# Optimization experiments

Hardware: AMD Instinct MI355X
Metric: run time of the kernel (lower is better)

Reference implementation:

```python
import jax, jax.numpy as jnp
import numpy as np

N_EMBD = 2048
N_HEAD = 16
HEAD_SIZE = N_EMBD // N_HEAD


def setup_inputs() -> dict:
    key = jax.random.key(0)
    k1, k2, k3 = jax.random.split(key, 3)
    x = jax.random.normal(k1, (4, 2048, N_EMBD), dtype=jnp.float32)
    # Linear weights stored as (in, out) for x @ W
    scale = 1.0 / np.sqrt(N_EMBD)
    w_qkv = jax.random.normal(k2, (N_EMBD, 3 * N_EMBD), dtype=jnp.float32) * scale
    w_proj = jax.random.normal(k3, (N_EMBD, N_EMBD), dtype=jnp.float32) * scale
    return {"x": x, "w_qkv": w_qkv, "w_proj": w_proj}


def reference(x, w_qkv, w_proj):
    B, T, C = x.shape
    qkv = x @ w_qkv  # [B, T, 3C]
    q, k, v = jnp.split(qkv, 3, axis=-1)
    # [B, H, T, Dh]
    def heads(t):
        return t.reshape(B, T, N_HEAD, HEAD_SIZE).transpose(0, 2, 1, 3)
    q, k, v = heads(q), heads(k), heads(v)
    scores = jnp.einsum('bhqd,bhkd->bhqk', q, k) * (1.0 / np.sqrt(HEAD_SIZE))
    causal = jnp.tril(jnp.ones((T, T), dtype=bool))
    scores = jnp.where(causal, scores, jnp.finfo(scores.dtype).min)
    att = jax.nn.softmax(scores, axis=-1)
    y = jnp.einsum('bhqk,bhkd->bhqd', att, v)
    y = y.transpose(0, 2, 1, 3).reshape(B, T, C)
    return y @ w_proj
```

## Files before the change

kernel.cpp:

```cpp
#include <hip/hip_runtime.h>

typedef unsigned short u16;
typedef unsigned int u32;
typedef __bf16 bf16x8 __attribute__((ext_vector_type(8)));
typedef float f32x4 __attribute__((ext_vector_type(4)));
typedef u32 u32x4 __attribute__((ext_vector_type(4)));

__device__ __forceinline__ u16 f2bf(float f) {
  u32 u = __builtin_bit_cast(u32, f);
  return (u16)((u + 0x7fffu + ((u >> 16) & 1u)) >> 16);
}

__device__ __forceinline__ f32x4 mfma16(bf16x8 a, bf16x8 b, f32x4 c) {
  return __builtin_amdgcn_mfma_f32_16x16x32_bf16(a, b, c, 0, 0, 0);
}

__device__ __forceinline__ u32 cvtpk_bf16(float lo, float hi) {
  u32 r;
  asm("v_cvt_pk_bf16_f32 %0, %1, %2" : "=v"(r) : "v"(lo), "v"(hi));
  return r;
}

struct alignas(8) U16x4 { u16 x, y, z, w; };

#define AS1 __attribute__((address_space(1)))
#define AS3 __attribute__((address_space(3)))
__device__ __forceinline__ void gl16(const u16* g, u16* l) {
  __builtin_amdgcn_global_load_lds((const AS1 u32*)g, (AS3 u32*)l, 16, 0, 0);
}

__global__ __launch_bounds__(256) void k_f32_to_bf16(const float* __restrict__ in,
                                                     u16* __restrict__ out, long n4) {
  long i = (long)blockIdx.x * blockDim.x + threadIdx.x;
  long stride = (long)gridDim.x * blockDim.x;
  for (; i < n4; i += stride) {
    float4 v = ((const float4*)in)[i];
    U16x4 o{f2bf(v.x), f2bf(v.y), f2bf(v.z), f2bf(v.w)};
    ((U16x4*)out)[i] = o;
  }
}

__global__ __launch_bounds__(256) void k_transpose_f32_to_bf16(const float* __restrict__ in,
                                                               u16* __restrict__ out,
                                                               int rows, int cols) {
  __shared__ float tile[32][33];
  int bc = blockIdx.x * 32, br = blockIdx.y * 32;
  int tx = threadIdx.x, ty = threadIdx.y;
  for (int i = 0; i < 32; i += 8)
    tile[ty + i][tx] = in[(long)(br + ty + i) * cols + bc + tx];
  __syncthreads();
  for (int i = 0; i < 32; i += 8)
    out[(long)(bc + ty + i) * rows + br + tx] = f2bf(tile[tx][ty + i]);
}

__global__ __launch_bounds__(256) void k_transpose_v(const u16* __restrict__ qkv,
                                                     u16* __restrict__ vt) {
  __shared__ u16 tile[32][33];
  int bh = blockIdx.z; int b = bh >> 4, h = bh & 15;
  int t0 = blockIdx.y * 32, d0 = blockIdx.x * 32;
  int tx = threadIdx.x, ty = threadIdx.y;
  const u16* src = qkv + (long)(b * 2048) * 6144 + 4096 + h * 128;
  for (int i = 0; i < 32; i += 8)
    tile[ty + i][tx] = src[(long)(t0 + ty + i) * 6144 + d0 + tx];
  __syncthreads();
  u16* dst = vt + (long)bh * 128 * 2048;
  for (int i = 0; i < 32; i += 8)
    dst[(long)(d0 + ty + i) * 2048 + t0 + tx] = tile[tx][ty + i];
}

template <typename OutT>
__global__ __launch_bounds__(512, 2) void k_gemm256(const u16* __restrict__ A,
                                                    const u16* __restrict__ Bt,
                                                    OutT* __restrict__ C,
                                                    int M, int N, int K) {
  __shared__ alignas(16) u16 As[4][8192];
  __shared__ alignas(16) u16 Bs[4][8192];

  int gx = gridDim.x;
  int nwg = gx * gridDim.y;
  int bid = blockIdx.y * gx + blockIdx.x;
  int swz = (bid & 7) * (nwg >> 3) + (bid >> 3);
  int rem = swz % (gx * 4);
  int bx = rem >> 2;
  int by = (swz / (gx * 4)) * 4 + (rem & 3);

  int tid = threadIdx.x;
  int lane = tid & 63;
  int w = tid >> 6;
  int wr = w >> 2, wc = w & 3;
  int lr = lane & 15, lg = lane >> 4;
  long brow = (long)by * 256, bcol = (long)bx * 256;

  int rS[2], cS[2];
#pragma unroll
  for (int i = 0; i < 2; ++i) {
    int q = i * 512 + tid;
    rS[i] = q >> 2;
    cS[i] = ((q & 3) ^ ((rS[i] >> 1) & 3)) << 3;
  }
  const u16* Ab = A + brow * K;
  const u16* Bb = Bt + bcol * K;

  int offA[8], offB[4];
#pragma unroll
  for (int m = 0; m < 8; ++m) {
    int row = wr * 128 + m * 16 + lr;
    offA[m] = row * 32 + ((lg ^ ((row >> 1) & 3)) << 3);
  }
#pragma unroll
  for (int n = 0; n < 4; ++n) {
    int row = wc * 64 + n * 16 + lr;
    offB[n] = row * 32 + ((lg ^ ((row >> 1) & 3)) << 3);
  }

  f32x4 zero = {0.f, 0.f, 0.f, 0.f};
  f32x4 acc[8][4];
#pragma unroll
  for (int m = 0; m < 8; ++m)
#pragma unroll
    for (int n = 0; n < 4; ++n) acc[m][n] = zero;

  int NS = K >> 5;

#define STAGE256(SBUF, KT)                                                          \
  do {                                                                              \
    int kk_ = (KT) << 5;                                                            \
    gl16(Ab + (long)rS[0] * K + kk_ + cS[0], &As[SBUF][(0 * 512 + w * 64) * 8]);    \
    gl16(Ab + (long)rS[1] * K + kk_ + cS[1], &As[SBUF][(1 * 512 + w * 64) * 8]);    \
    gl16(Bb + (long)rS[0] * K + kk_ + cS[0], &Bs[SBUF][(0 * 512 + w * 64) * 8]);    \
    gl16(Bb + (long)rS[1] * K + kk_ + cS[1], &Bs[SBUF][(1 * 512 + w * 64) * 8]);    \
  } while (0)

  STAGE256(0, 0);
  STAGE256(1, 1);
  STAGE256(2, 2);
  asm volatile("s_waitcnt vmcnt(8)" ::: "memory");
  __builtin_amdgcn_s_barrier();

  for (int s = 0; s < NS; ++s) {
    int cb = s & 3;
    bf16x8 af[8], bfn[4];
#pragma unroll
    for (int m = 0; m < 8; ++m) af[m] = *(const bf16x8*)&As[cb][offA[m]];
#pragma unroll
    for (int n = 0; n < 4; ++n) bfn[n] = *(const bf16x8*)&Bs[cb][offB[n]];
    int t = s + 3;
    int tb = t & 3;
    if (t > NS - 1) t = NS - 1;
    STAGE256(tb, t);
    __builtin_amdgcn_s_setprio(1);
#pragma unroll
    for (int m = 0; m < 4; ++m)
#pragma unroll
      for (int n = 0; n < 4; ++n) acc[m][n] = mfma16(af[m], bfn[n], acc[m][n]);
    __builtin_amdgcn_s_setprio(0);
    __builtin_amdgcn_s_setprio(1);
#pragma unroll
    for (int m = 4; m < 8; ++m)
#pragma unroll
      for (int n = 0; n < 4; ++n) acc[m][n] = mfma16(af[m], bfn[n], acc[m][n]);
    __builtin_amdgcn_s_setprio(0);
    asm volatile("s_waitcnt vmcnt(8)" ::: "memory");
    __builtin_amdgcn_s_barrier();
  }
#undef STAGE256
  asm volatile("s_waitcnt vmcnt(0)" ::: "memory");

#pragma unroll
  for (int m = 0; m < 8; ++m)
#pragma unroll
    for (int n = 0; n < 4; ++n)
#pragma unroll
      for (int r = 0; r < 4; ++r) {
        long row = brow + wr * 128 + m * 16 + lg * 4 + r;
        long col = bcol + wc * 64 + n * 16 + lr;
        float v = acc[m][n][r];
        if constexpr (sizeof(OutT) == 2)
          C[row * N + col] = (OutT)f2bf(v);
        else
          C[row * N + col] = v;
      }
}

__global__ __launch_bounds__(256, 2) void k_attn2(const u16* __restrict__ qkv,
                                                  const u16* __restrict__ vt,
                                                  u16* __restrict__ y) {
  __shared__ alignas(16) u16 Ks[2][64 * 128];
  __shared__ alignas(16) u16 Vs[2][128 * 64];

  int bh = blockIdx.x;
  int qb = 15 - (int)blockIdx.y;
  int b = bh >> 4, h = bh & 15;
  int tid = threadIdx.x;
  int lane = tid & 63;
  int w = tid >> 6;
  int lr = lane & 15, lg = lane >> 4;
  int x7 = lr & 7;
  bool hiA = (lane & 32) != 0;
  bool hiB = (lane & 16) != 0;
  const float scale = 0.08838834764831845f;

  const u16* kbase = qkv + (long)(b * 2048) * 6144 + 2048 + h * 128;
  const u16* vtbh = vt + (long)bh * 128 * 2048;
  int qbase = qb * 128 + w * 32;

  const u16* qptr = qkv + (long)(qb * 128 + b * 2048) * 6144 + h * 128;
  bf16x8 qf[2][4];
  for (int qsub = 0; qsub < 2; ++qsub)
    for (int dc = 0; dc < 4; ++dc)
      qf[qsub][dc] = *(const bf16x8*)(qptr + (long)(w * 32 + qsub * 16 + lr) * 6144 + dc * 32 + lg * 8);

  f32x4 zero = {0.f, 0.f, 0.f, 0.f};
  f32x4 o[2][8];
  for (int qs = 0; qs < 2; ++qs)
    for (int ds = 0; ds < 8; ++ds) o[qs][ds] = zero;
  float m_run[2] = {-1e30f, -1e30f};
  float l_run[2] = {0.f, 0.f};

  int nkt = 2 * qb + 2;
  int qmaxw = qbase + 31;

#define STAGE(BUF, KT)                                                          \
  do {                                                                          \
    for (int i_ = 0; i_ < 4; ++i_) {                                            \
      int rl_ = w * 16 + i_ * 4;                                                \
      int row_ = rl_ + (lane >> 4);                                             \
      int ch_ = (lane & 15) ^ (row_ & 7);                                       \
      gl16(kbase + (long)((KT)*64 + row_) * 6144 + ch_ * 8, &Ks[BUF][rl_ * 128]); \
    }                                                                           \
    for (int i_ = 0; i_ < 4; ++i_) {                                            \
      int dl_ = w * 32 + i_ * 8;                                                \
      int d_ = dl_ + (lane >> 3);                                               \
      int ch_ = (lane & 7) ^ (d_ & 7);                                          \
      gl16(vtbh + (long)d_ * 2048 + (KT)*64 + ch_ * 8, &Vs[BUF][dl_ * 64]);     \
    }                                                                           \
  } while (0)

#define COMPUTE(BUF, KT)                                                        \
  do {                                                                          \
    const u16* Kb = &Ks[BUF][0];                                                \
    const u16* Vb = &Vs[BUF][0];                                                \
    f32x4 s[2][4];                                                              \
    for (int qs = 0; qs < 2; ++qs)                                              \
      for (int ks = 0; ks < 4; ++ks) s[qs][ks] = zero;                          \
    for (int ks = 0; ks < 4; ++ks) {                                            \
      int row = ks * 16 + lr;                                                   \
      for (int dc = 0; dc < 4; ++dc) {                                          \
        bf16x8 kf = *(const bf16x8*)(Kb + row * 128 + ((dc * 4 + lg) ^ x7) * 8); \
        s[0][ks] = mfma16(kf, qf[0][dc], s[0][ks]);                             \
        s[1][ks] = mfma16(kf, qf[1][dc], s[1][ks]);                             \
      }                                                                         \
    }                                                                           \
    bf16x8 pa[2][2];                                                            \
    for (int qs = 0; qs < 2; ++qs) {                                            \
      int qg = qbase + qs * 16 + lr;                                            \
      float p[16];                                                              \
      float tmax = -1e30f;                                                      \
      for (int ks = 0; ks < 4; ++ks)                                            \
        for (int r = 0; r < 4; ++r) {                                           \
          int key = (KT)*64 + ks * 16 + lg * 4 + r;                             \
          float v = (key <= qg) ? s[qs][ks][r] * scale : -1e30f;                \
          p[ks * 4 + r] = v;                                                    \
          tmax = fmaxf(tmax, v);                                                \
        }                                                                       \
      tmax = fmaxf(tmax, __shfl_xor(tmax, 16));                                 \
      tmax = fmaxf(tmax, __shfl_xor(tmax, 32));                                 \
      float m_new = fmaxf(m_run[qs], tmax);                                     \
      float alpha = __expf(m_run[qs] - m_new);                                  \
      float psum = 0.f;                                                         \
      for (int i = 0; i < 16; ++i) {                                            \
        p[i] = __expf(p[i] - m_new);                                            \
        psum += p[i];                                                           \
      }                                                                         \
      psum += __shfl_xor(psum, 16);                                             \
      psum += __shfl_xor(psum, 32);                                             \
      l_run[qs] = l_run[qs] * alpha + psum;                                     \
      m_run[qs] = m_new;                                                        \
       \
       \
      for (int j = 0; j < 2; ++j) {                                             \
        u32 w0 = cvtpk_bf16(p[j * 8 + 0], p[j * 8 + 1]);                        \
        u32 w1 = cvtpk_bf16(p[j * 8 + 2], p[j * 8 + 3]);                        \
        u32 w2 = cvtpk_bf16(p[j * 8 + 4], p[j * 8 + 5]);                        \
        u32 w3 = cvtpk_bf16(p[j * 8 + 6], p[j * 8 + 7]);                        \
        u32 a0 = hiA ? w0 : w2, a1 = hiA ? w1 : w3;                             \
        u32 r0 = __shfl_xor(a0, 32), r1 = __shfl_xor(a1, 32);                   \
        u32 q0 = hiA ? r0 : w0, q1 = hiA ? r1 : w1;                             \
        u32 q2 = hiA ? w2 : r0, q3 = hiA ? w3 : r1;                             \
        u32 s0 = hiB ? q0 : q2, s1 = hiB ? q1 : q3;                             \
        u32 t0 = __shfl_xor(s0, 16), t1 = __shfl_xor(s1, 16);                   \
        u32x4 fw;                                                               \
        fw[0] = hiB ? t0 : q0;                                                  \
        fw[1] = hiB ? t1 : q1;                                                  \
        fw[2] = hiB ? q2 : t0;                                                  \
        fw[3] = hiB ? q3 : t1;                                                  \
        pa[qs][j] = __builtin_bit_cast(bf16x8, fw);                             \
      }                                                                         \
      float alr[4];                                                             \
      for (int r = 0; r < 4; ++r) alr[r] = __shfl(alpha, lg * 4 + r);           \
      for (int ds = 0; ds < 8; ++ds)                                            \
        for (int r = 0; r < 4; ++r) o[qs][ds][r] *= alr[r];                     \
    }                                                                           \
    for (int j = 0; j < 2; ++j) {                                               \
      int chv = ((j * 4 + lg) ^ x7) * 8;                                        \
      for (int ds = 0; ds < 8; ++ds) {                                          \
        bf16x8 vf = *(const bf16x8*)(Vb + (ds * 16 + lr) * 64 + chv);           \
        o[0][ds] = mfma16(pa[0][j], vf, o[0][ds]);                              \
        o[1][ds] = mfma16(pa[1][j], vf, o[1][ds]);                              \
      }                                                                         \
    }                                                                           \
  } while (0)

  int buf = 0;
  STAGE(0, 0);
  asm volatile("s_waitcnt vmcnt(0)" ::: "memory");
  __builtin_amdgcn_s_barrier();
  for (int kt = 0; kt < nkt - 1; ++kt) {
    STAGE(buf ^ 1, kt + 1);
    if (kt * 64 <= qmaxw) COMPUTE(buf, kt);
    asm volatile("s_waitcnt vmcnt(0) lgkmcnt(0)" ::: "memory");
    __builtin_amdgcn_s_barrier();
    buf ^= 1;
  }
  {
    int kt = nkt - 1;
    if (kt * 64 <= qmaxw) COMPUTE(buf, kt);
  }
#undef STAGE
#undef COMPUTE

  float linv[2][4];
  for (int qs = 0; qs < 2; ++qs)
    for (int r = 0; r < 4; ++r) linv[qs][r] = 1.0f / __shfl(l_run[qs], lg * 4 + r);
  u16* yb = y + (long)(b * 2048 + qb * 128 + w * 32) * 2048 + h * 128;
  for (int qs = 0; qs < 2; ++qs)
    for (int ds = 0; ds < 8; ++ds)
      for (int r = 0; r < 4; ++r)
        yb[(long)(qs * 16 + lg * 4 + r) * 2048 + ds * 16 + lr] = f2bf(o[qs][ds][r] * linv[qs][r]);
}

extern "C" void kernel_launch(void* const* d_in, const int* in_sizes, int n_in,
                              void* d_out, int out_size, void* d_ws, size_t ws_size,
                              hipStream_t stream) {
  const float* x = (const float*)d_in[0];
  const float* w_qkv = (const float*)d_in[1];
  const float* w_proj = (const float*)d_in[2];
  float* out = (float*)d_out;

  char* ws = (char*)d_ws;
  if (ws_size < 201326592ull) return;
  u16* QKV = (u16*)(ws);
  u16* WqT = (u16*)(ws + 100663296);
  u16* WpT = (u16*)(ws + 125829120);
  u16* Xb  = (u16*)(ws + 134217728);
  u16* Vt  = (u16*)(ws + 167772160);

  dim3 tb32x8(32, 8);

  k_f32_to_bf16<<<2048, 256, 0, stream>>>(x, Xb, (8192L * 2048) / 4);
  k_transpose_f32_to_bf16<<<dim3(192, 64), tb32x8, 0, stream>>>(w_qkv, WqT, 2048, 6144);
  k_transpose_f32_to_bf16<<<dim3(64, 64), tb32x8, 0, stream>>>(w_proj, WpT, 2048, 2048);

  k_gemm256<u16><<<dim3(24, 32), 512, 0, stream>>>(Xb, WqT, QKV, 8192, 6144, 2048);

  k_transpose_v<<<dim3(4, 64, 64), tb32x8, 0, stream>>>(QKV, Vt);

  k_attn2<<<dim3(64, 16), 256, 0, stream>>>(QKV, Vt, Xb );

  k_gemm256<float><<<dim3(8, 32), 512, 0, stream>>>(Xb, WpT, out, 8192, 2048, 2048);
}
```

Measured before the change: 422.9 us.

## Split K and V staging so attention waits only on the tile it needs

Splits the attention tile load into separate K and V stages and the compute into a QK/softmax part and a PV part. Partial vmcnt waits let the QK phase start once K has landed while V is still loading, instead of waiting for all outstanding loads each iteration. In exchange it adds a second barrier per key tile and issues one redundant load on the final iteration.

```diff
diff --git a/kernel.cpp b/kernel.cpp
--- a/kernel.cpp
+++ b/kernel.cpp
@@ -220,7 +220,7 @@
   int nkt = 2 * qb + 2;
   int qmaxw = qbase + 31;
 
-#define STAGE(BUF, KT)                                                          \
+#define STAGE_K(BUF, KT)                                                        \
   do {                                                                          \
     for (int i_ = 0; i_ < 4; ++i_) {                                            \
       int rl_ = w * 16 + i_ * 4;                                                \
@@ -228,6 +228,10 @@
       int ch_ = (lane & 15) ^ (row_ & 7);                                       \
       gl16(kbase + (long)((KT)*64 + row_) * 6144 + ch_ * 8, &Ks[BUF][rl_ * 128]); \
     }                                                                           \
+  } while (0)
+
+#define STAGE_V(BUF, KT)                                                        \
+  do {                                                                          \
     for (int i_ = 0; i_ < 4; ++i_) {                                            \
       int dl_ = w * 32 + i_ * 8;                                                \
       int d_ = dl_ + (lane >> 3);                                               \
@@ -236,10 +240,9 @@
     }                                                                           \
   } while (0)
 
-#define COMPUTE(BUF, KT)                                                        \
+#define QKPART(BUF, KT, PA)                                                     \
   do {                                                                          \
     const u16* Kb = &Ks[BUF][0];                                                \
-    const u16* Vb = &Vs[BUF][0];                                                \
     f32x4 s[2][4];                                                              \
     for (int qs = 0; qs < 2; ++qs)                                              \
       for (int ks = 0; ks < 4; ++ks) s[qs][ks] = zero;                          \
@@ -251,7 +254,6 @@
         s[1][ks] = mfma16(kf, qf[1][dc], s[1][ks]);                             \
       }                                                                         \
     }                                                                           \
-    bf16x8 pa[2][2];                                                            \
     for (int qs = 0; qs < 2; ++qs) {                                            \
       int qg = qbase + qs * 16 + lr;                                            \
       float p[16];                                                              \
@@ -294,40 +296,52 @@
         fw[1] = hiB ? t1 : q1;                                                  \
         fw[2] = hiB ? q2 : t0;                                                  \
         fw[3] = hiB ? q3 : t1;                                                  \
-        pa[qs][j] = __builtin_bit_cast(bf16x8, fw);                             \
+        PA[qs][j] = __builtin_bit_cast(bf16x8, fw);                             \
       }                                                                         \
       float alr[4];                                                             \
       for (int r = 0; r < 4; ++r) alr[r] = __shfl(alpha, lg * 4 + r);           \
       for (int ds = 0; ds < 8; ++ds)                                            \
         for (int r = 0; r < 4; ++r) o[qs][ds][r] *= alr[r];                     \
     }                                                                           \
+  } while (0)
+
+#define PVPART(BUF, PA)                                                         \
+  do {                                                                          \
+    const u16* Vb = &Vs[BUF][0];                                                \
     for (int j = 0; j < 2; ++j) {                                               \
       int chv = ((j * 4 + lg) ^ x7) * 8;                                        \
       for (int ds = 0; ds < 8; ++ds) {                                          \
         bf16x8 vf = *(const bf16x8*)(Vb + (ds * 16 + lr) * 64 + chv);           \
-        o[0][ds] = mfma16(pa[0][j], vf, o[0][ds]);                              \
-        o[1][ds] = mfma16(pa[1][j], vf, o[1][ds]);                              \
+        o[0][ds] = mfma16(PA[0][j], vf, o[0][ds]);                              \
+        o[1][ds] = mfma16(PA[1][j], vf, o[1][ds]);                              \
       }                                                                         \
     }                                                                           \
   } while (0)
 
-  int buf = 0;
-  STAGE(0, 0);
+  STAGE_K(0, 0);
+  STAGE_V(0, 0);
+  asm volatile("s_waitcnt vmcnt(4)" ::: "memory");
+  __builtin_amdgcn_s_barrier();
+
+  for (int t = 0; t < nkt; ++t) {
+    int tn = (t + 1 < nkt) ? t + 1 : nkt - 1;
+    int nb = (t + 1) & 1;
+    bool live = (t * 64 <= qmaxw);
+    bf16x8 pa[2][2];
+    STAGE_K(nb, tn);
+    if (live) QKPART(t & 1, t, pa);
+    STAGE_V(nb, tn);
+    asm volatile("s_waitcnt vmcnt(8)" ::: "memory");
+    __builtin_amdgcn_s_barrier();
+    if (live) PVPART(t & 1, pa);
+    asm volatile("s_waitcnt vmcnt(4)" ::: "memory");
+    __builtin_amdgcn_s_barrier();
+  }
   asm volatile("s_waitcnt vmcnt(0)" ::: "memory");
-  __builtin_amdgcn_s_barrier();
-  for (int kt = 0; kt < nkt - 1; ++kt) {
-    STAGE(buf ^ 1, kt + 1);
-    if (kt * 64 <= qmaxw) COMPUTE(buf, kt);
-    asm volatile("s_waitcnt vmcnt(0) lgkmcnt(0)" ::: "memory");
-    __builtin_amdgcn_s_barrier();
-    buf ^= 1;
-  }
-  {
-    int kt = nkt - 1;
-    if (kt * 64 <= qmaxw) COMPUTE(buf, kt);
-  }
-#undef STAGE
-#undef COMPUTE
+#undef STAGE_K
+#undef STAGE_V
+#undef QKPART
+#undef PVPART
 
   float linv[2][4];
   for (int qs = 0; qs < 2; ++qs)
```

New measurement: 418.8 us. No clear change (-1.0%).
